# Performance work log

Hardware: AMD Instinct MI355X
Metric: run time of the kernel (lower is better)

Reference implementation:

```python
import jax, jax.numpy as jnp
import numpy as np

B, S, H = 2, 2048, 896
NH, NKV, HD = 14, 2, 64        # heads, kv heads, head_dim
GROUPS = NH // NKV             # 7
ROPE_THETA = 1000000.0


def rotate_half(x):
    x1 = x[..., : x.shape[-1] // 2]
    x2 = x[..., x.shape[-1] // 2:]
    return jnp.concatenate([-x2, x1], axis=-1)


def rope_tables(seq_len):
    inv_freq = 1.0 / ROPE_THETA ** (jnp.arange(0, HD, 2, dtype=jnp.float32) / HD)
    t = jnp.arange(seq_len, dtype=jnp.float32)
    freqs = jnp.outer(t, inv_freq)            # [S, HD/2]
    emb = jnp.concatenate([freqs, freqs], -1)  # [S, HD]
    return jnp.cos(emb), jnp.sin(emb)


def setup_inputs() -> dict:
    key = jax.random.key(0)
    ks = jax.random.split(key, 8)
    sc = 0.02
    hidden_states = jax.random.normal(ks[0], (B, S, H), jnp.float32)
    causal = jnp.tril(jnp.ones((S, S), jnp.bool_))
    attention_mask = jnp.where(causal, 0.0, -1e9).astype(jnp.float32)[None, None]
    return {
        "hidden_states": hidden_states,
        "attention_mask": attention_mask,
        "Wq": jax.random.normal(ks[1], (H, NH * HD), jnp.float32) * sc,
        "bq": jnp.zeros((NH * HD,), jnp.float32),
        "Wk": jax.random.normal(ks[2], (H, NKV * HD), jnp.float32) * sc,
        "bk": jnp.zeros((NKV * HD,), jnp.float32),
        "Wv": jax.random.normal(ks[3], (H, NKV * HD), jnp.float32) * sc,
        "bv": jnp.zeros((NKV * HD,), jnp.float32),
        "Wo": jax.random.normal(ks[4], (H, H), jnp.float32) * sc,
    }


def reference(hidden_states, attention_mask, Wq, bq, Wk, bk, Wv, bv, Wo):
    b, s, _ = hidden_states.shape
    q = (hidden_states @ Wq + bq).reshape(b, s, NH, HD).transpose(0, 2, 1, 3)   # [b,nh,s,hd]
    k = (hidden_states @ Wk + bk).reshape(b, s, NKV, HD).transpose(0, 2, 1, 3)  # [b,nkv,s,hd]
    v = (hidden_states @ Wv + bv).reshape(b, s, NKV, HD).transpose(0, 2, 1, 3)
    cos, sin = rope_tables(s)                 # position_offset = 0
    cos = cos[None, None]; sin = sin[None, None]
    q = q * cos + rotate_half(q) * sin
    k = k * cos + rotate_half(k) * sin
    # GQA: expand kv heads to full heads (matches jnp.repeat on axis=1)
    k = jnp.repeat(k, GROUPS, axis=1)
    v = jnp.repeat(v, GROUPS, axis=1)
    scores = jnp.einsum('bhqd,bhkd->bhqk', q, k) / np.sqrt(HD).astype(np.float32)
    scores = scores + attention_mask
    attn = jax.nn.softmax(scores, axis=-1)
    out = jnp.einsum('bhqk,bhkd->bhqd', attn, v)
    out = out.transpose(0, 2, 1, 3).reshape(b, s, NH * HD)
    return out @ Wo
```

## Files before the change

### kernel.cpp

```cpp
#include <hip/hip_runtime.h>

#define S_LEN 2048
#define NHEADS 14
#define NKVH 2
#define HDIM 64
#define HID 896
#define NQKV 1152
#define NCHUNK 40

typedef __bf16 bf16;
typedef __bf16 bf16x4 __attribute__((ext_vector_type(4)));
typedef __bf16 bf16x8 __attribute__((ext_vector_type(8)));
typedef float f32x4 __attribute__((ext_vector_type(4)));
typedef unsigned int u32x4 __attribute__((ext_vector_type(4)));

__device__ inline f32x4 mfma16(bf16x8 a, bf16x8 b, f32x4 c) {
  return __builtin_amdgcn_mfma_f32_16x16x32_bf16(a, b, c, 0, 0, 0);
}

__device__ inline void gload_lds16(const bf16* g, bf16* l) {
  __builtin_amdgcn_global_load_lds(
      (const __attribute__((address_space(1))) void*)g,
      (__attribute__((address_space(3))) void*)l, 16, 0, 0);
}
__device__ inline void gload_lds16b(const void* g, void* l) {
  __builtin_amdgcn_global_load_lds(
      (const __attribute__((address_space(1))) void*)g,
      (__attribute__((address_space(3))) void*)l, 16, 0, 0);
}

__device__ inline unsigned cvtpk(float lo, float hi) {
  unsigned r;
  asm("v_cvt_pk_bf16_f32 %0, %1, %2" : "=v"(r) : "v"(lo), "v"(hi));
  return r;
}

__device__ inline void chunk_map(int c, int& qt, int& ch) {
  if (c < 4)       { qt = c;                ch = 0; }
  else if (c < 12) { qt = 4 + ((c - 4) >> 1); ch = (c - 4) & 1; }
  else if (c < 24) { int d = c - 12; qt = 8 + d / 3; ch = d % 3; }
  else             { int d = c - 24; qt = 12 + (d >> 2); ch = d & 3; }
}

__global__ __launch_bounds__(256) void prep_kernel(
    const float* __restrict__ X, bf16* __restrict__ Xb,
    const float* __restrict__ Wq, const float* __restrict__ Wk,
    const float* __restrict__ Wv, const float* __restrict__ Wo,
    bf16* __restrict__ WqkvT, bf16* __restrict__ WoT,
    const float* __restrict__ bq, const float* __restrict__ bk,
    const float* __restrict__ bv, float* __restrict__ biasq) {
  __shared__ float tile[32][33];
  int blk = blockIdx.x;
  int tid = threadIdx.x;
  if (blk < 3584) {
    int i = blk * 256 + tid;
    if (i < 917504) {
      float4 v = reinterpret_cast<const float4*>(X)[i];
      bf16x4 o;
      o[0] = (bf16)v.x; o[1] = (bf16)v.y; o[2] = (bf16)v.z; o[3] = (bf16)v.w;
      reinterpret_cast<bf16x4*>(Xb)[i] = o;
    }
    return;
  }
  if (blk < 5376) {
    int t = blk - 3584;
    const float* W; bf16* dst; int N, bx, by;
    if (t < 784)       { W = Wq; dst = WqkvT;                      N = 896; bx = t % 28;          by = t / 28; }
    else if (t < 896)  { int u = t - 784;  W = Wk; dst = WqkvT + (size_t)896 * 896;  N = 128; bx = u % 4; by = u / 4; }
    else if (t < 1008) { int u = t - 896;  W = Wv; dst = WqkvT + (size_t)1024 * 896; N = 128; bx = u % 4; by = u / 4; }
    else               { int u = t - 1008; W = Wo; dst = WoT;      N = 896; bx = u % 28;          by = u / 28; }
    int n0 = bx * 32, k0 = by * 32;
    int tx = tid & 31, ty = tid >> 5;
#pragma unroll
    for (int j = 0; j < 32; j += 8)
      tile[ty + j][tx] = W[(size_t)(k0 + ty + j) * N + n0 + tx];
    __syncthreads();
#pragma unroll
    for (int j = 0; j < 32; j += 8)
      dst[(size_t)(n0 + ty + j) * HID + k0 + tx] = (bf16)tile[tx][ty + j];
    return;
  }
  int i = (blk - 5376) * 256 + tid;
  if (i < 896) biasq[i] = bq[i];
  else if (i < 1024) biasq[i] = bk[i - 896];
  else if (i < 1152) biasq[i] = bv[i - 1024];
}

__global__ __launch_bounds__(256) void gemm_bt_kernel(const bf16* __restrict__ A,
                                                      const bf16* __restrict__ Bt,
                                                      const float* __restrict__ bias,
                                                      float* __restrict__ C,
                                                      int M, int N, int K) {
  __shared__ __align__(16) bf16 As[2][128][32];
  __shared__ __align__(16) bf16 Bs[2][64][32];
  int n0 = blockIdx.x * 64, m0 = blockIdx.y * 128;
  int tid = threadIdx.x;
  int wid = tid >> 6, lane = tid & 63;
  int lr = lane & 15, lh = lane >> 4;
  int wr = wid >> 1, wc = wid & 1;
  f32x4 acc[4][2] = {};

  auto stage = [&](int buf, int k0) {
#pragma unroll
    for (int i = 0; i < 2; ++i) {
      int seg = i * 4 + wid;
      int idx = seg * 512 + lane * 8;
      int r = idx >> 5, c = idx & 31;
      gload_lds16(A + (size_t)(m0 + r) * K + k0 + c, &As[buf][0][0] + seg * 512);
    }
    {
      int idx = wid * 512 + lane * 8;
      int r = idx >> 5, c = idx & 31;
      gload_lds16(Bt + (size_t)(n0 + r) * K + k0 + c, &Bs[buf][0][0] + wid * 512);
    }
  };

  stage(0, 0);
  __syncthreads();
  int nk = K >> 5;
  int cur = 0;
  for (int t = 0; t < nk; ++t) {
    if (t + 1 < nk) stage(cur ^ 1, (t + 1) << 5);
    bf16x8 am[4], bn[2];
#pragma unroll
    for (int mf = 0; mf < 4; ++mf)
      am[mf] = *reinterpret_cast<const bf16x8*>(&As[cur][wr * 64 + mf * 16 + lr][lh * 8]);
#pragma unroll
    for (int nf = 0; nf < 2; ++nf)
      bn[nf] = *reinterpret_cast<const bf16x8*>(&Bs[cur][wc * 32 + nf * 16 + lr][lh * 8]);
    __builtin_amdgcn_s_setprio(1);
#pragma unroll
    for (int mf = 0; mf < 4; ++mf)
#pragma unroll
      for (int nf = 0; nf < 2; ++nf)
        acc[mf][nf] = mfma16(am[mf], bn[nf], acc[mf][nf]);
    __builtin_amdgcn_s_setprio(0);
    __syncthreads();
    cur ^= 1;
  }

#pragma unroll
  for (int nf = 0; nf < 2; ++nf) {
    int col = n0 + wc * 32 + nf * 16 + lr;
    float b = bias ? bias[col] : 0.f;
#pragma unroll
    for (int mf = 0; mf < 4; ++mf) {
      int row0 = m0 + wr * 64 + mf * 16 + lh * 4;
#pragma unroll
      for (int j = 0; j < 4; ++j)
        C[(size_t)(row0 + j) * N + col] = acc[mf][nf][j] + b;
    }
  }
}

__global__ __launch_bounds__(256) void rope_kernel(const float* __restrict__ QKV,
                                                   bf16* __restrict__ Qb,
                                                   bf16* __restrict__ Kb,
                                                   bf16* __restrict__ Vt) {
  int t = blockIdx.x;
  int b = t >> 11, s = t & (S_LEN - 1);
  const float* row = QKV + (size_t)t * NQKV;
  int tid = threadIdx.x;
  __shared__ float cs[32], sn[32];
  if (tid < 32) {
    float inv = expf(-(float)tid * (13.815510557964274f / 32.0f));
    float a = (float)s * inv;
    float c, si;
    sincosf(a, &si, &c);
    cs[tid] = c; sn[tid] = si;
  }
  __syncthreads();
  const float QSCALE = 0.125f * 1.44269504088896f;
  for (int p = tid; p < NHEADS * 32; p += 256) {
    int h = p >> 5, d = p & 31;
    float v1 = row[h * 64 + d], v2 = row[h * 64 + d + 32];
    float c = cs[d], si = sn[d];
    size_t base = ((size_t)(b * NHEADS + h) * S_LEN + s) * HDIM;
    Qb[base + d]      = (bf16)((v1 * c - v2 * si) * QSCALE);
    Qb[base + d + 32] = (bf16)((v2 * c + v1 * si) * QSCALE);
  }
  if (tid < NKVH * 32) {
    int kh = tid >> 5, d = tid & 31;
    float v1 = row[896 + kh * 64 + d], v2 = row[896 + kh * 64 + d + 32];
    float c = cs[d], si = sn[d];
    size_t base = ((size_t)(b * NKVH + kh) * S_LEN + s) * HDIM;
    int sw = (((s & 7) ^ ((s >> 3) & 1)) << 3);
    Kb[base + (d ^ sw)]        = (bf16)(v1 * c - v2 * si);
    Kb[base + ((d + 32) ^ sw)] = (bf16)(v2 * c + v1 * si);
  }
  if (tid < NKVH * 64) {
    int kh = tid >> 6, d = tid & 63;
    float v = row[1024 + tid];
    int col = (s & ~63) | ((s & 63) ^ ((d & 7) << 3));
    Vt[((size_t)(b * NKVH + kh) * HDIM + d) * S_LEN + col] = (bf16)v;
  }
}

__global__ __launch_bounds__(256, 4) void attn_kernel(const bf16* __restrict__ Qb,
                                                      const bf16* __restrict__ Kb,
                                                      const bf16* __restrict__ Vt,
                                                      bf16* __restrict__ Opart,
                                                      float* __restrict__ Oml) {
  int blk = blockIdx.x;
  int c = (NCHUNK - 1) - (blk % NCHUNK), bh = blk / NCHUNK;
  int qt, ch;
  chunk_map(c, qt, ch);
  int h = bh % NHEADS, b = bh / NHEADS;
  int q0 = qt * 128;
  int kv = h / 7;
  int kc0 = ch * 512;
  int kend = min(kc0 + 512, q0 + 128);
  int nt = (kend - kc0) >> 6;
  int tid = threadIdx.x, wid = tid >> 6, lane = tid & 63;
  int lr = lane & 15, lh = lane >> 4;
  int swk = (lr & 7) << 4;

  const bf16* Qp = Qb + ((size_t)(b * NHEADS + h) * S_LEN + q0 + wid * 32) * HDIM;
  const char* KpB = (const char*)(Kb + (size_t)(b * NKVH + kv) * S_LEN * HDIM);
  const char* VpB = (const char*)(Vt + (size_t)(b * NKVH + kv) * HDIM * S_LEN);

  __shared__ __align__(16) bf16 Ks[2][4096];
  __shared__ __align__(16) bf16 Vs[2][4096];

  bf16x8 aq[2][2];
#pragma unroll
  for (int f = 0; f < 2; ++f)
#pragma unroll
    for (int kk = 0; kk < 2; ++kk)
      aq[f][kk] = *reinterpret_cast<const bf16x8*>(
          Qp + (size_t)(f * 16 + lr) * HDIM + kk * 32 + lh * 8);

  float m[2] = {-3.0e38f, -3.0e38f}, l[2] = {0.f, 0.f};
  f32x4 o[2][4] = {};

  auto stage = [&](int buf, int kv0) {
#pragma unroll
    for (int i = 0; i < 2; ++i) {
      gload_lds16b(KpB + (size_t)kv0 * 128 + wid * 2048 + i * 1024 + lane * 16,
                   &Ks[buf][wid * 1024 + i * 512]);
      int d = wid * 16 + i * 8 + (lane >> 3);
      gload_lds16b(VpB + (size_t)d * (S_LEN * 2) + kv0 * 2 + (lane & 7) * 16,
                   &Vs[buf][wid * 1024 + i * 512]);
    }
  };

  stage(0, kc0);
  __syncthreads();

  int qf0 = q0 + wid * 32;
  int cur = 0;
  for (int t = 0; t < nt; ++t) {
    int kv0 = kc0 + (t << 6);
    const char* KsB = (const char*)&Ks[cur][0];
    f32x4 sacc[2][4] = {};
#pragma unroll
    for (int nf = 0; nf < 4; ++nf) {
      int rowk = 8 * (lr >> 2) + (lr & 3) + ((nf & 1) << 2) + ((nf >> 1) << 5);
      int rsw = (((rowk & 7) ^ ((rowk >> 3) & 1)) << 4);
#pragma unroll
      for (int kk = 0; kk < 2; ++kk) {
        bf16x8 kb = *(const bf16x8*)(KsB + rowk * 128 + ((kk * 64 + lh * 16) ^ rsw));
        sacc[0][nf] = mfma16(kb, aq[0][kk], sacc[0][nf]);
        sacc[1][nf] = mfma16(kb, aq[1][kk], sacc[1][nf]);
      }
    }
    if (t + 1 < nt) stage(cur ^ 1, kv0 + 64);

    float mx[2];
#pragma unroll
    for (int f = 0; f < 2; ++f) {
      int qg = qf0 + f * 16 + lr;
      if (kv0 + 63 > qf0 + f * 16) {
#pragma unroll
        for (int nf = 0; nf < 4; ++nf) {
          int kb0 = kv0 + ((nf & 1) << 2) + ((nf >> 1) << 5) + (lh << 3);
#pragma unroll
          for (int j = 0; j < 4; ++j)
            if (kb0 + j > qg) sacc[f][nf][j] = -3.0e38f;
        }
      }
      f32x4 m4 = sacc[f][0];
#pragma unroll
      for (int nf = 1; nf < 4; ++nf)
#pragma unroll
        for (int j = 0; j < 4; ++j) m4[j] = fmaxf(m4[j], sacc[f][nf][j]);
      float mxl = fmaxf(fmaxf(m4[0], m4[1]), fmaxf(m4[2], m4[3]));
      mxl = fmaxf(mxl, __shfl_xor(mxl, 16));
      mxl = fmaxf(mxl, __shfl_xor(mxl, 32));
      mx[f] = mxl;
    }
    float g = fmaxf(mx[0] - m[0], mx[1] - m[1]);
    if (!__all(g <= 8.0f)) {
#pragma unroll
      for (int f = 0; f < 2; ++f) {
        float mn = fmaxf(m[f], mx[f]);
        float al = exp2f(m[f] - mn);
        m[f] = mn;
        l[f] *= al;
        f32x4 av;
#pragma unroll
        for (int j = 0; j < 4; ++j) av[j] = __shfl(al, (lh << 2) + j);
#pragma unroll
        for (int nf = 0; nf < 4; ++nf) o[f][nf] *= av;
      }
    }
    bf16x8 pa[2][2];
#pragma unroll
    for (int f = 0; f < 2; ++f) {
      f32x4 rs4 = {0.f, 0.f, 0.f, 0.f};
#pragma unroll
      for (int nf = 0; nf < 4; ++nf) {
#pragma unroll
        for (int j = 0; j < 4; ++j)
          sacc[f][nf][j] = exp2f(sacc[f][nf][j] - m[f]);
        rs4 += sacc[f][nf];
      }
      float rsum = (rs4[0] + rs4[1]) + (rs4[2] + rs4[3]);
      rsum += __shfl_xor(rsum, 16);
      rsum += __shfl_xor(rsum, 32);
      l[f] += rsum;
#pragma unroll
      for (int kk = 0; kk < 2; ++kk) {
        u32x4 w;
        w[0] = cvtpk(sacc[f][2 * kk][0], sacc[f][2 * kk][1]);
        w[1] = cvtpk(sacc[f][2 * kk][2], sacc[f][2 * kk][3]);
        w[2] = cvtpk(sacc[f][2 * kk + 1][0], sacc[f][2 * kk + 1][1]);
        w[3] = cvtpk(sacc[f][2 * kk + 1][2], sacc[f][2 * kk + 1][3]);
        pa[f][kk] = __builtin_bit_cast(bf16x8, w);
      }
    }
    const char* VsB = (const char*)&Vs[cur][0];
#pragma unroll
    for (int nf = 0; nf < 4; ++nf) {
#pragma unroll
      for (int kk = 0; kk < 2; ++kk) {
        bf16x8 vb = *(const bf16x8*)(VsB + (nf * 16 + lr) * 128 + ((kk * 64 + lh * 16) ^ swk));
        o[0][nf] = mfma16(pa[0][kk], vb, o[0][nf]);
        o[1][nf] = mfma16(pa[1][kk], vb, o[1][nf]);
      }
    }
    __syncthreads();
    cur ^= 1;
  }

  size_t pbase = ((size_t)bh * NCHUNK + c) * (128 * 64);
#pragma unroll
  for (int f = 0; f < 2; ++f)
#pragma unroll
    for (int nf = 0; nf < 4; ++nf) {
      int col = nf * 16 + lr;
#pragma unroll
      for (int j = 0; j < 4; ++j) {
        int rloc = wid * 32 + f * 16 + (lh << 2) + j;
        Opart[pbase + (size_t)rloc * 64 + col] = (bf16)o[f][nf][j];
      }
    }
  if (lane < 16) {
    size_t mbase = ((size_t)bh * NCHUNK + c) * 128;
#pragma unroll
    for (int f = 0; f < 2; ++f) {
      int rloc = wid * 32 + f * 16 + lane;
      Oml[(mbase + rloc) * 2]     = m[f];
      Oml[(mbase + rloc) * 2 + 1] = l[f];
    }
  }
}

__global__ __launch_bounds__(256) void combine_kernel(const bf16* __restrict__ Opart,
                                                      const float* __restrict__ Oml,
                                                      bf16* __restrict__ Ob) {
  int blk = blockIdx.x;
  int qt = blk & 15, bh = blk >> 4;
  int h = bh % NHEADS, b = bh / NHEADS;
  int a = qt >> 2, bb = qt & 3;
  int nch = a + 1;
  int coff = (a + 1) * (2 * a + bb);
  int t = threadIdx.x;
  int row = t >> 1, cg = t & 1;

  float M = -__builtin_inff();
  for (int i = 0; i < nch; ++i)
    M = fmaxf(M, Oml[(((size_t)bh * NCHUNK + coff + i) * 128 + row) * 2]);
  float L = 0.f;
  for (int i = 0; i < nch; ++i) {
    size_t mb = (((size_t)bh * NCHUNK + coff + i) * 128 + row) * 2;
    L += exp2f(Oml[mb] - M) * Oml[mb + 1];
  }
  float acc[32];
#pragma unroll
  for (int k = 0; k < 32; ++k) acc[k] = 0.f;
  for (int i = 0; i < nch; ++i) {
    size_t mb = (((size_t)bh * NCHUNK + coff + i) * 128 + row) * 2;
    float w = exp2f(Oml[mb] - M);
    const bf16* src = Opart + (((size_t)bh * NCHUNK + coff + i) * 128 + row) * 64 + cg * 32;
#pragma unroll
    for (int v = 0; v < 4; ++v) {
      bf16x8 x = *reinterpret_cast<const bf16x8*>(src + v * 8);
#pragma unroll
      for (int k = 0; k < 8; ++k) acc[v * 8 + k] += w * (float)x[k];
    }
  }
  float inv = 1.0f / L;
  bf16* dst = Ob + ((size_t)(b * S_LEN) + qt * 128 + row) * HID + h * 64 + cg * 32;
#pragma unroll
  for (int v = 0; v < 4; ++v) {
    bf16x8 r;
#pragma unroll
    for (int k = 0; k < 8; ++k) r[k] = (bf16)(acc[v * 8 + k] * inv);
    *reinterpret_cast<bf16x8*>(dst + v * 8) = r;
  }
}

extern "C" void kernel_launch(void* const* d_in, const int* in_sizes, int n_in,
                              void* d_out, int out_size, void* d_ws, size_t ws_size,
                              hipStream_t stream) {
  (void)in_sizes; (void)n_in; (void)out_size; (void)ws_size;
  const float* X  = (const float*)d_in[0];
  const float* Wq = (const float*)d_in[2];
  const float* bq = (const float*)d_in[3];
  const float* Wk = (const float*)d_in[4];
  const float* bk = (const float*)d_in[5];
  const float* Wv = (const float*)d_in[6];
  const float* bv = (const float*)d_in[7];
  const float* Wo = (const float*)d_in[8];
  float* OUT = (float*)d_out;

  char* ws = (char*)d_ws;
  bf16*  Xb    = (bf16*)(ws);
  bf16*  WqkvT = (bf16*)(ws + 7340032);
  bf16*  WoT   = (bf16*)(ws + 9404416);
  float* biasq = (float*)(ws + 11010048);
  float* QKV   = (float*)(ws + 11014656);
  bf16*  Qbuf  = (bf16*)(ws + 29889024);
  bf16*  Kbuf  = (bf16*)(ws + 37229056);
  bf16*  Vbuf  = (bf16*)(ws + 38277632);
  bf16*  Opart = (bf16*)(ws + 11014656);
  float* Oml   = (float*)(ws + 7340032);
  bf16*  Obuf  = Xb;

  prep_kernel<<<5381, 256, 0, stream>>>(X, Xb, Wq, Wk, Wv, Wo, WqkvT, WoT,
                                        bq, bk, bv, biasq);
  gemm_bt_kernel<<<dim3(18, 32), 256, 0, stream>>>(Xb, WqkvT, biasq, QKV, 4096, 1152, 896);
  rope_kernel<<<4096, 256, 0, stream>>>(QKV, Qbuf, Kbuf, Vbuf);
  attn_kernel<<<28 * NCHUNK, 256, 0, stream>>>(Qbuf, Kbuf, Vbuf, Opart, Oml);
  combine_kernel<<<28 * 16, 256, 0, stream>>>(Opart, Oml, Obuf);
  gemm_bt_kernel<<<dim3(14, 32), 256, 0, stream>>>(Obuf, WoT, nullptr, OUT, 4096, 896, 896);
}
```

Baseline: 113.0 us.

## Fuse RoPE and QKV layout scatter into the QKV GEMM epilogue

```diff
diff --git a/kernel.cpp b/kernel.cpp
--- a/kernel.cpp
+++ b/kernel.cpp
@@ -48,7 +48,8 @@
     const float* __restrict__ Wv, const float* __restrict__ Wo,
     bf16* __restrict__ WqkvT, bf16* __restrict__ WoT,
     const float* __restrict__ bq, const float* __restrict__ bk,
-    const float* __restrict__ bv, float* __restrict__ biasq) {
+    const float* __restrict__ bv, float* __restrict__ biasq,
+    float* __restrict__ trig) {
   __shared__ float tile[32][33];
   int blk = blockIdx.x;
   int tid = threadIdx.x;
@@ -80,15 +81,158 @@
       dst[(size_t)(n0 + ty + j) * HID + k0 + tx] = (bf16)tile[tx][ty + j];
     return;
   }
-  int i = (blk - 5376) * 256 + tid;
-  if (i < 896) biasq[i] = bq[i];
-  else if (i < 1024) biasq[i] = bk[i - 896];
-  else if (i < 1152) biasq[i] = bv[i - 1024];
+  if (blk < 5381) {
+    int i = (blk - 5376) * 256 + tid;
+    if (i < 896) biasq[i] = bq[i];
+    else if (i < 1024) biasq[i] = bk[i - 896];
+    else if (i < 1152) biasq[i] = bv[i - 1024];
+    return;
+  }
+  {
+    int ti = blk - 5381;
+    int s = ti * 8 + (tid >> 5);
+    int d = tid & 31;
+    float inv = expf(-(float)d * (13.815510557964274f / 32.0f));
+    float a = (float)s * inv;
+    float c, si;
+    sincosf(a, &si, &c);
+    trig[(size_t)s * 64 + d] = c;
+    trig[(size_t)s * 64 + 32 + d] = si;
+  }
+}
+
+__global__ __launch_bounds__(256) void gemm_qkv_kernel(const bf16* __restrict__ A,
+                                                       const bf16* __restrict__ Bt,
+                                                       const float* __restrict__ bias,
+                                                       const float* __restrict__ trig,
+                                                       bf16* __restrict__ Qb,
+                                                       bf16* __restrict__ Kb,
+                                                       bf16* __restrict__ Vt) {
+  __shared__ __align__(16) char smem[33280];
+  bf16* As = (bf16*)smem;
+  bf16* Bs = (bf16*)(smem + 16384);
+  float* tileO = (float*)smem;
+  const int K = 896;
+  int n0 = blockIdx.x * 64, m0 = blockIdx.y * 128;
+  int tid = threadIdx.x;
+  int wid = tid >> 6, lane = tid & 63;
+  int lr = lane & 15, lh = lane >> 4;
+  int wr = wid >> 1, wc = wid & 1;
+  f32x4 acc[4][2] = {};
+
+  auto stage = [&](int buf, int k0) {
+#pragma unroll
+    for (int i = 0; i < 2; ++i) {
+      int seg = i * 4 + wid;
+      int idx = seg * 512 + lane * 8;
+      int r = idx >> 5, c = idx & 31;
+      gload_lds16(A + (size_t)(m0 + r) * K + k0 + c, As + buf * 4096 + seg * 512);
+    }
+    {
+      int idx = wid * 512 + lane * 8;
+      int r = idx >> 5, c = idx & 31;
+      gload_lds16(Bt + (size_t)(n0 + r) * K + k0 + c, Bs + buf * 2048 + wid * 512);
+    }
+  };
+
+  stage(0, 0);
+  __syncthreads();
+  int nk = K >> 5;
+  int cur = 0;
+  for (int t = 0; t < nk; ++t) {
+    if (t + 1 < nk) stage(cur ^ 1, (t + 1) << 5);
+    bf16x8 am[4], bn[2];
+#pragma unroll
+    for (int mf = 0; mf < 4; ++mf)
+      am[mf] = *reinterpret_cast<const bf16x8*>(As + cur * 4096 + (wr * 64 + mf * 16 + lr) * 32 + lh * 8);
+#pragma unroll
+    for (int nf = 0; nf < 2; ++nf)
+      bn[nf] = *reinterpret_cast<const bf16x8*>(Bs + cur * 2048 + (wc * 32 + nf * 16 + lr) * 32 + lh * 8);
+    __builtin_amdgcn_s_setprio(1);
+#pragma unroll
+    for (int mf = 0; mf < 4; ++mf)
+#pragma unroll
+      for (int nf = 0; nf < 2; ++nf)
+        acc[mf][nf] = mfma16(am[mf], bn[nf], acc[mf][nf]);
+    __builtin_amdgcn_s_setprio(0);
+    __syncthreads();
+    cur ^= 1;
+  }
+
+#pragma unroll
+  for (int nf = 0; nf < 2; ++nf) {
+    int col = wc * 32 + nf * 16 + lr;
+    float bb = bias[n0 + col];
+#pragma unroll
+    for (int mf = 0; mf < 4; ++mf) {
+      int row0 = wr * 64 + mf * 16 + lh * 4;
+#pragma unroll
+      for (int j = 0; j < 4; ++j)
+        tileO[(row0 + j) * 65 + col] = acc[mf][nf][j] + bb;
+    }
+  }
+  __syncthreads();
+
+  const float QSCALE = 0.125f * 1.44269504088896f;
+  int b = blockIdx.y >> 4;
+  int s0 = (blockIdx.y & 15) * 128;
+  int bx = blockIdx.x;
+  if (bx < 14) {
+    int r2 = tid >> 1, half = tid & 1;
+    int s = s0 + r2;
+    const float* tr = trig + (size_t)s * 64;
+    size_t base = ((size_t)(b * NHEADS + bx) * S_LEN + s) * HDIM;
+    bf16x8 o1[2], o2[2];
+#pragma unroll
+    for (int v = 0; v < 2; ++v)
+#pragma unroll
+      for (int p = 0; p < 8; ++p) {
+        int d = half * 16 + v * 8 + p;
+        float c = tr[d], sn = tr[32 + d];
+        float v1 = tileO[r2 * 65 + d], v2 = tileO[r2 * 65 + d + 32];
+        o1[v][p] = (bf16)((v1 * c - v2 * sn) * QSCALE);
+        o2[v][p] = (bf16)((v2 * c + v1 * sn) * QSCALE);
+      }
+    *(bf16x8*)(Qb + base + half * 16)      = o1[0];
+    *(bf16x8*)(Qb + base + half * 16 + 8)  = o1[1];
+    *(bf16x8*)(Qb + base + 32 + half * 16)     = o2[0];
+    *(bf16x8*)(Qb + base + 32 + half * 16 + 8) = o2[1];
+  } else if (bx < 16) {
+    int kh = bx - 14;
+    int r2 = tid >> 1, half = tid & 1;
+    int s = s0 + r2;
+    const float* tr = trig + (size_t)s * 64;
+    int sw = (((s & 7) ^ ((s >> 3) & 1)) << 3);
+    size_t base = ((size_t)(b * NKVH + kh) * S_LEN + s) * HDIM;
+#pragma unroll
+    for (int p = 0; p < 16; ++p) {
+      int d = half * 16 + p;
+      float c = tr[d], sn = tr[32 + d];
+      float v1 = tileO[r2 * 65 + d], v2 = tileO[r2 * 65 + d + 32];
+      Kb[base + (d ^ sw)]        = (bf16)(v1 * c - v2 * sn);
+      Kb[base + ((d + 32) ^ sw)] = (bf16)(v2 * c + v1 * sn);
+    }
+  } else {
+    int kh = bx - 16;
+    int d = tid & 63, seg = tid >> 6;
+    size_t vbase = ((size_t)(b * NKVH + kh) * HDIM + d) * S_LEN;
+    int c8 = (d & 7) << 3;
+#pragma unroll
+    for (int g = 0; g < 4; ++g) {
+      int sl = seg * 32 + g * 8;
+      bf16x8 w;
+#pragma unroll
+      for (int p = 0; p < 8; ++p)
+        w[p] = (bf16)tileO[(sl + p) * 65 + d];
+      int s = s0 + sl;
+      int col = (s & ~63) | (((s & 63) ^ c8) & ~7);
+      *(bf16x8*)(Vt + vbase + col) = w;
+    }
+  }
 }
 
 __global__ __launch_bounds__(256) void gemm_bt_kernel(const bf16* __restrict__ A,
                                                       const bf16* __restrict__ Bt,
-                                                      const float* __restrict__ bias,
                                                       float* __restrict__ C,
                                                       int M, int N, int K) {
   __shared__ __align__(16) bf16 As[2][128][32];
@@ -142,57 +286,13 @@
 #pragma unroll
   for (int nf = 0; nf < 2; ++nf) {
     int col = n0 + wc * 32 + nf * 16 + lr;
-    float b = bias ? bias[col] : 0.f;
 #pragma unroll
     for (int mf = 0; mf < 4; ++mf) {
       int row0 = m0 + wr * 64 + mf * 16 + lh * 4;
 #pragma unroll
       for (int j = 0; j < 4; ++j)
-        C[(size_t)(row0 + j) * N + col] = acc[mf][nf][j] + b;
-    }
-  }
-}
-
-__global__ __launch_bounds__(256) void rope_kernel(const float* __restrict__ QKV,
-                                                   bf16* __restrict__ Qb,
-                                                   bf16* __restrict__ Kb,
-                                                   bf16* __restrict__ Vt) {
-  int t = blockIdx.x;
-  int b = t >> 11, s = t & (S_LEN - 1);
-  const float* row = QKV + (size_t)t * NQKV;
-  int tid = threadIdx.x;
-  __shared__ float cs[32], sn[32];
-  if (tid < 32) {
-    float inv = expf(-(float)tid * (13.815510557964274f / 32.0f));
-    float a = (float)s * inv;
-    float c, si;
-    sincosf(a, &si, &c);
-    cs[tid] = c; sn[tid] = si;
-  }
-  __syncthreads();
-  const float QSCALE = 0.125f * 1.44269504088896f;
-  for (int p = tid; p < NHEADS * 32; p += 256) {
-    int h = p >> 5, d = p & 31;
-    float v1 = row[h * 64 + d], v2 = row[h * 64 + d + 32];
-    float c = cs[d], si = sn[d];
-    size_t base = ((size_t)(b * NHEADS + h) * S_LEN + s) * HDIM;
-    Qb[base + d]      = (bf16)((v1 * c - v2 * si) * QSCALE);
-    Qb[base + d + 32] = (bf16)((v2 * c + v1 * si) * QSCALE);
-  }
-  if (tid < NKVH * 32) {
-    int kh = tid >> 5, d = tid & 31;
-    float v1 = row[896 + kh * 64 + d], v2 = row[896 + kh * 64 + d + 32];
-    float c = cs[d], si = sn[d];
-    size_t base = ((size_t)(b * NKVH + kh) * S_LEN + s) * HDIM;
-    int sw = (((s & 7) ^ ((s >> 3) & 1)) << 3);
-    Kb[base + (d ^ sw)]        = (bf16)(v1 * c - v2 * si);
-    Kb[base + ((d + 32) ^ sw)] = (bf16)(v2 * c + v1 * si);
-  }
-  if (tid < NKVH * 64) {
-    int kh = tid >> 6, d = tid & 63;
-    float v = row[1024 + tid];
-    int col = (s & ~63) | ((s & 63) ^ ((d & 7) << 3));
-    Vt[((size_t)(b * NKVH + kh) * HDIM + d) * S_LEN + col] = (bf16)v;
+        C[(size_t)(row0 + j) * N + col] = acc[mf][nf][j];
+    }
   }
 }
 
@@ -430,19 +530,19 @@
   bf16*  WqkvT = (bf16*)(ws + 7340032);
   bf16*  WoT   = (bf16*)(ws + 9404416);
   float* biasq = (float*)(ws + 11010048);
-  float* QKV   = (float*)(ws + 11014656);
+  bf16*  Opart = (bf16*)(ws + 11014656);
+  float* trig  = (float*)(ws + 29364736);
   bf16*  Qbuf  = (bf16*)(ws + 29889024);
   bf16*  Kbuf  = (bf16*)(ws + 37229056);
   bf16*  Vbuf  = (bf16*)(ws + 38277632);
-  bf16*  Opart = (bf16*)(ws + 11014656);
   float* Oml   = (float*)(ws + 7340032);
   bf16*  Obuf  = Xb;
 
-  prep_kernel<<<5381, 256, 0, stream>>>(X, Xb, Wq, Wk, Wv, Wo, WqkvT, WoT,
-                                        bq, bk, bv, biasq);
-  gemm_bt_kernel<<<dim3(18, 32), 256, 0, stream>>>(Xb, WqkvT, biasq, QKV, 4096, 1152, 896);
-  rope_kernel<<<4096, 256, 0, stream>>>(QKV, Qbuf, Kbuf, Vbuf);
+  prep_kernel<<<5637, 256, 0, stream>>>(X, Xb, Wq, Wk, Wv, Wo, WqkvT, WoT,
+                                        bq, bk, bv, biasq, trig);
+  gemm_qkv_kernel<<<dim3(18, 32), 256, 0, stream>>>(Xb, WqkvT, biasq, trig,
+                                                    Qbuf, Kbuf, Vbuf);
   attn_kernel<<<28 * NCHUNK, 256, 0, stream>>>(Qbuf, Kbuf, Vbuf, Opart, Oml);
   combine_kernel<<<28 * 16, 256, 0, stream>>>(Opart, Oml, Obuf);
-  gemm_bt_kernel<<<dim3(14, 32), 256, 0, stream>>>(Obuf, WoT, nullptr, OUT, 4096, 896, 896);
-}
+  gemm_bt_kernel<<<dim3(14, 32), 256, 0, stream>>>(Obuf, WoT, OUT, 4096, 896, 896);
+}
```

New measurement: 106.8 us. 1.06x faster.
